# Kernel optimization log

Measured on AMD Instinct MI355X. Metric: run time of the kernel, lower is better.

The kernel has to match this reference:

```python
import jax, jax.numpy as jnp
import numpy as np

B, S, D, H = 2, 2048, 1024, 16
DK = D // H

def setup_inputs() -> dict:
    key = jax.random.key(0)
    ks = jax.random.split(key, 12)
    scale = 1.0 / np.sqrt(D)
    return {
        "q": jax.random.normal(ks[0], (B, S, D), jnp.float32),
        "k": jax.random.normal(ks[1], (B, S, D), jnp.float32),
        "v": jax.random.normal(ks[2], (B, S, D), jnp.float32),
        "mask": jax.random.randint(ks[3], (B, 1, S, S), 0, 2, jnp.int32),
        "w_q": jax.random.normal(ks[4], (D, D), jnp.float32) * scale,
        "b_q": jnp.zeros((D,), jnp.float32),
        "w_k": jax.random.normal(ks[5], (D, D), jnp.float32) * scale,
        "b_k": jnp.zeros((D,), jnp.float32),
        "w_v": jax.random.normal(ks[6], (D, D), jnp.float32) * scale,
        "b_v": jnp.zeros((D,), jnp.float32),
        "w_o": jax.random.normal(ks[7], (D, D), jnp.float32) * scale,
        "b_o": jnp.zeros((D,), jnp.float32),
    }

def reference(q, k, v, mask, w_q, b_q, w_k, b_k, w_v, b_v, w_o, b_o):
    # projections (nn.Linear: x @ W^T + b)
    Q = q @ w_q.T + b_q  # [B,S,D]
    K = k @ w_k.T + b_k
    V = v @ w_v.T + b_v
    # split heads -> [B,H,S,DK]
    Q = Q.reshape(B, S, H, DK).transpose(0, 2, 1, 3)
    K = K.reshape(B, S, H, DK).transpose(0, 2, 1, 3)
    V = V.reshape(B, S, H, DK).transpose(0, 2, 1, 3)
    scores = jnp.einsum("bhqd,bhkd->bhqk", Q, K) / jnp.sqrt(jnp.float32(DK))
    scores = jnp.where(mask == 0, jnp.float32(-1e9), scores)
    attn = jax.nn.softmax(scores, axis=-1)  # dropout p=0 -> identity
    x = jnp.einsum("bhqk,bhkd->bhqd", attn, V)
    x = x.transpose(0, 2, 1, 3).reshape(B, S, D)
    return x @ w_o.T + b_o
```

## Files before the change

### kernel.cpp

```cpp
#include <hip/hip_runtime.h>
#include <hip/hip_bf16.h>
#include <cstdint>
#include <cstddef>

typedef short bf16x8 __attribute__((ext_vector_type(8)));
typedef short bf16x4v __attribute__((ext_vector_type(4)));
typedef float f32x4 __attribute__((ext_vector_type(4)));
typedef __hip_bfloat16 bf16;

constexpr int Bb = 2, Ss = 2048, Dd = 1024, Hh = 16, DKk = 64;

__device__ __forceinline__ void async_lds16(void* lds, const void* g) {
  __builtin_amdgcn_global_load_lds(
      (const __attribute__((address_space(1))) void*)g,
      (__attribute__((address_space(3))) void*)lds, 16, 0, 0);
}

__device__ __forceinline__ float bf2f(bf16 x) { return __bfloat162float(x); }
__device__ __forceinline__ short f2bf(float x) {
  bf16 h = __float2bfloat16(x);
  return *(short*)&h;
}
__device__ __forceinline__ float bfs2f(short s) {
  return __uint_as_float(((uint32_t)(uint16_t)s) << 16);
}

struct CvtArgs {
  const float* src[12];
  short* dst[12];
  int n[12];
  int count;
};

__global__ __launch_bounds__(256)
void cvt_all(CvtArgs a)
{
  const int t = blockIdx.y;
  if (t >= a.count) return;
  const float* s = a.src[t];
  short* d = a.dst[t];
  const int n = a.n[t];
  const int stride = gridDim.x * blockDim.x * 4;
  for (int i = (blockIdx.x * blockDim.x + threadIdx.x) * 4; i < n; i += stride) {
    const float4 v = *(const float4*)(s + i);
    bf16x4v o;
    o[0] = f2bf(v.x); o[1] = f2bf(v.y); o[2] = f2bf(v.z); o[3] = f2bf(v.w);
    *(bf16x4v*)(d + i) = o;
  }
}

__global__ __launch_bounds__(256)
void pack_mask(const int* __restrict__ mask, uint32_t* __restrict__ bits)
{
  const int i = blockIdx.x * 256 + threadIdx.x;
  const unsigned long long bal = __ballot(mask[i] != 0);
  if ((threadIdx.x & 63) == 0)
    *(unsigned long long*)(bits + (i >> 5)) = bal;
}

__global__ __launch_bounds__(256, 2)
void gemm_bt(const bf16* __restrict__ A0, const bf16* __restrict__ A1, const bf16* __restrict__ A2,
             const bf16* __restrict__ W0, const bf16* __restrict__ W1, const bf16* __restrict__ W2,
             const bf16* __restrict__ b0, const bf16* __restrict__ b1, const bf16* __restrict__ b2,
             void* __restrict__ O0, void* __restrict__ O1, void* __restrict__ O2,
             float scale0, int wf32, int vtrans)
{
  extern __shared__ char smem[];
  const int mt  = blockIdx.x;
  const int by  = blockIdx.y;
  const int mat = by >> 3;
  const int nt  = by & 7;
  const bf16* A    = (mat == 0) ? A0 : (mat == 1) ? A1 : A2;
  const bf16* W    = (mat == 0) ? W0 : (mat == 1) ? W1 : W2;
  const bf16* bias = (mat == 0) ? b0 : (mat == 1) ? b1 : b2;
  void*       Out  = (mat == 0) ? O0 : (mat == 1) ? O1 : O2;
  const float scale = (mat == 0) ? scale0 : 1.0f;

  const int tid  = threadIdx.x;
  const int w    = tid >> 6;
  const int lane = tid & 63;
  const int quad = lane >> 4;
  const int l16  = lane & 15;
  const int wm   = (w & 1) * 64;
  const int wn   = (w >> 1) * 64;

  const int srow = lane >> 3;
  const int sseg = (lane & 7) ^ srow;

  const char* Abytes = (const char*)A;
  const char* Wbytes = (const char*)W;

  f32x4 acc[4][4];
#pragma unroll
  for (int i = 0; i < 4; ++i)
#pragma unroll
    for (int j = 0; j < 4; ++j) acc[i][j] = f32x4{0.f, 0.f, 0.f, 0.f};

  for (int kt = 0; kt < 16; ++kt) {
    __syncthreads();
#pragma unroll
    for (int c = 0; c < 4; ++c) {
      const int r0 = w * 32 + c * 8;
      async_lds16(smem + r0 * 128,
                  Abytes + (size_t)(mt * 128 + r0 + srow) * 2048 + kt * 128 + sseg * 16);
      async_lds16(smem + 16384 + r0 * 128,
                  Wbytes + (size_t)(nt * 128 + r0 + srow) * 2048 + kt * 128 + sseg * 16);
    }
    __syncthreads();
#pragma unroll
    for (int s = 0; s < 2; ++s) {
      bf16x8 af[4], bfg[4];
#pragma unroll
      for (int mb = 0; mb < 4; ++mb) {
        const int row = wm + mb * 16 + l16;
        af[mb] = *(const bf16x8*)(smem + row * 128 + (((4 * s + quad) ^ (row & 7)) * 16));
      }
#pragma unroll
      for (int nb = 0; nb < 4; ++nb) {
        const int row = wn + nb * 16 + l16;
        bfg[nb] = *(const bf16x8*)(smem + 16384 + row * 128 + (((4 * s + quad) ^ (row & 7)) * 16));
      }
#pragma unroll
      for (int mb = 0; mb < 4; ++mb)
#pragma unroll
        for (int nb = 0; nb < 4; ++nb)
          acc[mb][nb] = __builtin_amdgcn_mfma_f32_16x16x32_bf16(af[mb], bfg[nb], acc[mb][nb], 0, 0, 0);
    }
  }

  if (vtrans && mat == 2) {
    __syncthreads();
#pragma unroll
    for (int nb = 0; nb < 4; ++nb) {
      const int dk = wn + nb * 16 + l16;
      const float bv = bf2f(bias[nt * 128 + dk]);
#pragma unroll
      for (int mb = 0; mb < 4; ++mb) {
        const int s0 = wm + mb * 16 + quad * 4;
        bf16x4v pk;
#pragma unroll
        for (int r = 0; r < 4; ++r) pk[r] = f2bf(acc[mb][nb][r] + bv);
        *(bf16x4v*)(smem + dk * 256 + (((s0 >> 3) ^ (dk & 15)) * 16) + (s0 & 7) * 2) = pk;
      }
    }
    __syncthreads();
    const int bidx  = (mt * 128) >> 11;
    const int sbase = (mt * 128) & 2047;
#pragma unroll
    for (int i = 0; i < 8; ++i) {
      const int dk  = i * 16 + (tid >> 4);
      const int seg = tid & 15;
      bf16x8 vrow = *(const bf16x8*)(smem + dk * 256 + ((seg ^ (dk & 15)) * 16));
      *(bf16x8*)((bf16*)Out + (size_t)bidx * 2097152 + (size_t)(nt * 128 + dk) * 2048
                 + sbase + seg * 8) = vrow;
    }
  } else {
#pragma unroll
    for (int nb = 0; nb < 4; ++nb) {
      const int col = nt * 128 + wn + nb * 16 + l16;
      const float bv = bf2f(bias[col]);
#pragma unroll
      for (int mb = 0; mb < 4; ++mb) {
#pragma unroll
        for (int r = 0; r < 4; ++r) {
          const int row = mt * 128 + wm + mb * 16 + quad * 4 + r;
          const float val = (acc[mb][nb][r] + bv) * scale;
          const size_t idx = (size_t)row * 1024 + col;
          if (wf32) ((float*)Out)[idx] = val;
          else      ((bf16*)Out)[idx] = __float2bfloat16(val);
        }
      }
    }
  }
}

__global__ __launch_bounds__(256, 5)
void attn(const bf16* __restrict__ Qp, const bf16* __restrict__ Kp,
          const bf16* __restrict__ VpT, const uint32_t* __restrict__ mbits,
          bf16* __restrict__ Opart, float* __restrict__ Lpart)
{
  __shared__ char smem[32768];
  char* Pb = smem;
  char* Vt = smem + 16384;

  const int tile  = blockIdx.x;
  const int split = blockIdx.y;
  const int qt = tile & 31, h = (tile >> 5) & 15, b = tile >> 9;
  const int tid = threadIdx.x, w = tid >> 6, lane = tid & 63;
  const int quad = lane >> 4, l16 = lane & 15;
  const int qb = qt * 64;
  const size_t headoff = (size_t)b * (Ss * Dd) + h * DKk;
  const int qrow = qb + w * 16 + l16;

  bf16x8 qf[2];
#pragma unroll
  for (int s2 = 0; s2 < 2; ++s2)
    qf[s2] = *(const bf16x8*)(Qp + headoff + (size_t)qrow * Dd + s2 * 32 + quad * 8);

  f32x4 o[4];
  float Lacc = 0.f;
#pragma unroll
  for (int nbk = 0; nbk < 4; ++nbk) o[nbk] = f32x4{0.f, 0.f, 0.f, 0.f};

  const uint32_t* mrow = mbits + (size_t)(b * Ss + qrow) * 64;

  for (int kc = split * 8; kc < split * 8 + 8; ++kc) {
    const int kb = kc * 128;
    __syncthreads();
#pragma unroll
    for (int c = 0; c < 4; ++c) {
      {
        const int row = c * 32 + w * 8 + (lane >> 3);
        const int seg = (lane & 7) ^ (row & 7);
        async_lds16(Pb + c * 4096 + w * 1024,
                    Kp + headoff + (size_t)(kb + row) * Dd + seg * 8);
      }
      {
        const int row = c * 16 + w * 4 + (lane >> 4);
        const int seg = (lane & 15) ^ (row & 15);
        async_lds16(Vt + c * 4096 + w * 1024,
                    VpT + (size_t)b * 2097152 + (size_t)(h * 64 + row) * 2048 + kb + seg * 8);
      }
    }
    __syncthreads();

    f32x4 sc[8];
#pragma unroll
    for (int nb = 0; nb < 8; ++nb) sc[nb] = f32x4{0.f, 0.f, 0.f, 0.f};
#pragma unroll
    for (int s2 = 0; s2 < 2; ++s2)
#pragma unroll
      for (int nb = 0; nb < 8; ++nb) {
        const int row = nb * 16 + l16;
        bf16x8 kf = *(const bf16x8*)(Pb + row * 128 + (((s2 * 4 + quad) ^ (row & 7)) * 16));
        sc[nb] = __builtin_amdgcn_mfma_f32_16x16x32_bf16(kf, qf[s2], sc[nb], 0, 0, 0);
      }
    __syncthreads();

    const uint4 mwv = *(const uint4*)(mrow + kc * 4);
    const uint32_t mwa[4] = {mwv.x, mwv.y, mwv.z, mwv.w};
#pragma unroll
    for (int nb = 0; nb < 8; ++nb) {
      const uint32_t nib = (mwa[nb >> 1] >> ((nb & 1) * 16 + quad * 4)) & 0xFu;
      bf16x4v pk;
#pragma unroll
      for (int r = 0; r < 4; ++r) {
        const float p = (nib & (1u << r)) ? __expf(sc[nb][r]) : 0.0f;
        Lacc += p;
        pk[r] = f2bf(p);
      }
      *(bf16x4v*)(Pb + (size_t)(w * 16 + l16) * 256 +
                  (((2 * nb + (quad >> 1)) ^ l16) * 16) + (quad & 1) * 8) = pk;
    }
    asm volatile("s_waitcnt lgkmcnt(0)" ::: "memory");

#pragma unroll
    for (int kb4 = 0; kb4 < 2; ++kb4) {
      bf16x8 pf[2];
#pragma unroll
      for (int u = 0; u < 2; ++u)
        pf[u] = *(const bf16x8*)(Pb + (size_t)(w * 16 + l16) * 256 +
                                 (((kb4 * 8 + u * 4 + quad) ^ l16) * 16));
#pragma unroll
      for (int nbk = 0; nbk < 4; ++nbk) {
        const int row = nbk * 16 + l16;
#pragma unroll
        for (int u = 0; u < 2; ++u) {
          bf16x8 vf = *(const bf16x8*)(Vt + row * 256 +
                                       ((((kb4 * 2 + u) * 4 + quad) ^ (row & 15)) * 16));
          o[nbk] = __builtin_amdgcn_mfma_f32_16x16x32_bf16(pf[u], vf, o[nbk], 0, 0, 0);
        }
      }
    }
  }

  float Lq = Lacc;
  Lq += __shfl_xor(Lq, 16);
  Lq += __shfl_xor(Lq, 32);
  const size_t pbase = (size_t)(split * 1024 + tile) * 64;
#pragma unroll
  for (int r = 0; r < 4; ++r) {
    const int rr = w * 16 + quad * 4 + r;
#pragma unroll
    for (int nbk = 0; nbk < 4; ++nbk)
      Opart[(pbase + rr) * 64 + nbk * 16 + l16] = __float2bfloat16(o[nbk][r]);
  }
  if (quad == 0) Lpart[pbase + w * 16 + l16] = Lq;
}

__global__ __launch_bounds__(256)
void combine(const bf16* __restrict__ Opart, const float* __restrict__ Lpart,
             bf16* __restrict__ Xa)
{
  const int t = threadIdx.x;
  const int row = blockIdx.x * 32 + (t >> 3);
  const int dkc = (t & 7) * 8;
  const float L = Lpart[row] + Lpart[65536 + row];
  const float inv = 1.0f / L;
  const bf16x8 O0 = *(const bf16x8*)(Opart + (size_t)row * 64 + dkc);
  const bf16x8 O1 = *(const bf16x8*)(Opart + (size_t)(65536 + row) * 64 + dkc);
  bf16x8 res;
#pragma unroll
  for (int j = 0; j < 8; ++j)
    res[j] = f2bf((bfs2f(O0[j]) + bfs2f(O1[j])) * inv);
  const int tile = row >> 6, r64 = row & 63;
  const int b = tile >> 9, h = (tile >> 5) & 15, q = (tile & 31) * 64 + r64;
  *(bf16x8*)(Xa + (size_t)(b * 2048 + q) * 1024 + h * 64 + dkc) = res;
}

extern "C" void kernel_launch(void* const* d_in, const int* in_sizes, int n_in,
                              void* d_out, int out_size, void* d_ws, size_t ws_size,
                              hipStream_t stream)
{
  const float* q  = (const float*)d_in[0];
  const float* k  = (const float*)d_in[1];
  const float* v  = (const float*)d_in[2];
  const int*   mk = (const int*)d_in[3];
  const float* wq = (const float*)d_in[4];
  const float* bq = (const float*)d_in[5];
  const float* wk = (const float*)d_in[6];
  const float* bk = (const float*)d_in[7];
  const float* wv = (const float*)d_in[8];
  const float* bv = (const float*)d_in[9];
  const float* wo = (const float*)d_in[10];
  const float* bo = (const float*)d_in[11];
  float* out = (float*)d_out;

  char* ws = (char*)d_ws;
  bf16* qb_  = (bf16*)(ws + ((size_t)0  << 20));
  bf16* kb_  = (bf16*)(ws + ((size_t)8  << 20));
  bf16* vb_  = (bf16*)(ws + ((size_t)16 << 20));
  bf16* Qp   = (bf16*)(ws + ((size_t)24 << 20));
  bf16* Kp   = (bf16*)(ws + ((size_t)32 << 20));
  bf16* VpT  = (bf16*)(ws + ((size_t)40 << 20));
  bf16* wqb  = (bf16*)(ws + ((size_t)48 << 20));
  bf16* wkb  = (bf16*)(ws + ((size_t)50 << 20));
  bf16* wvb  = (bf16*)(ws + ((size_t)52 << 20));
  bf16* wob  = (bf16*)(ws + ((size_t)54 << 20));
  bf16* bqb  = (bf16*)(ws + ((size_t)56 << 20));
  bf16* bkb  = (bf16*)(ws + ((size_t)56 << 20) + 2048);
  bf16* bvb  = (bf16*)(ws + ((size_t)56 << 20) + 4096);
  bf16* bob  = (bf16*)(ws + ((size_t)56 << 20) + 6144);
  uint32_t* mbits = (uint32_t*)(ws + ((size_t)56 << 20) + 65536);
  bf16*  Opart = (bf16*)(ws + ((size_t)0 << 20));
  float* Lpart = (float*)(ws + ((size_t)16 << 20));
  bf16*  Xa    = (bf16*)(ws + ((size_t)17 << 20));

  const int NA = Bb * Ss * Dd;
  const int NW = Dd * Dd;

  CvtArgs ca;
  ca.src[0] = q;  ca.dst[0] = (short*)qb_; ca.n[0] = NA;
  ca.src[1] = k;  ca.dst[1] = (short*)kb_; ca.n[1] = NA;
  ca.src[2] = v;  ca.dst[2] = (short*)vb_; ca.n[2] = NA;
  ca.src[3] = wq; ca.dst[3] = (short*)wqb; ca.n[3] = NW;
  ca.src[4] = wk; ca.dst[4] = (short*)wkb; ca.n[4] = NW;
  ca.src[5] = wv; ca.dst[5] = (short*)wvb; ca.n[5] = NW;
  ca.src[6] = wo; ca.dst[6] = (short*)wob; ca.n[6] = NW;
  ca.src[7] = bq; ca.dst[7] = (short*)bqb; ca.n[7] = Dd;
  ca.src[8] = bk; ca.dst[8] = (short*)bkb; ca.n[8] = Dd;
  ca.src[9] = bv; ca.dst[9] = (short*)bvb; ca.n[9] = Dd;
  ca.src[10] = bo; ca.dst[10] = (short*)bob; ca.n[10] = Dd;
  ca.src[11] = bo; ca.dst[11] = (short*)bob; ca.n[11] = 0;
  ca.count = 11;

  dim3 blk(256);
  cvt_all<<<dim3(1024, 11), blk, 0, stream>>>(ca);
  pack_mask<<<dim3(Bb * Ss * Ss / 256), blk, 0, stream>>>(mk, mbits);

  gemm_bt<<<dim3(32, 24), blk, 32768, stream>>>(qb_, kb_, vb_, wqb, wkb, wvb,
                                                bqb, bkb, bvb,
                                                (void*)Qp, (void*)Kp, (void*)VpT,
                                                0.125f, 0, 1);
  attn<<<dim3(1024, 2), blk, 0, stream>>>(Qp, Kp, VpT, mbits, Opart, Lpart);
  combine<<<dim3(2048), blk, 0, stream>>>(Opart, Lpart, Xa);
  gemm_bt<<<dim3(32, 8), blk, 32768, stream>>>(Xa, Xa, Xa, wob, wob, wob,
                                               bob, bob, bob,
                                               (void*)out, (void*)out, (void*)out,
                                               1.0f, 1, 0);
}
```

Measured before the change: 296.7 us.

## Process 128 query rows per attention block with a three-way KV split

Each attention block now covers 128 query rows, with each wave handling two 16-row sets. Every K and V tile loaded into LDS therefore feeds twice as many MFMAs, and the key range is split three ways (6/5/5 chunks) instead of two. The combine kernel sums three partials, and the workspace is remapped to fit the larger partial buffers. The bf16 conversions now use a cheap add-and-shift rounding, and the gemm launch bounds allow three blocks per CU. The trade-off is more registers and more LDS per block (48KB), which lowers occupancy, plus a third partial to write and read.

```diff
diff --git a/kernel.cpp b/kernel.cpp
--- a/kernel.cpp
+++ b/kernel.cpp
@@ -20,6 +20,13 @@
 __device__ __forceinline__ short f2bf(float x) {
   bf16 h = __float2bfloat16(x);
   return *(short*)&h;
+}
+__device__ __forceinline__ short f2bf_fast(float x) {
+  return (short)((__float_as_uint(x) + 0x8000u) >> 16);
+}
+__device__ __forceinline__ uint32_t pack2bf(float a, float b) {
+  return ((__float_as_uint(a) + 0x8000u) >> 16) |
+         ((__float_as_uint(b) + 0x8000u) & 0xffff0000u);
 }
 __device__ __forceinline__ float bfs2f(short s) {
   return __uint_as_float(((uint32_t)(uint16_t)s) << 16);
@@ -58,7 +65,7 @@
     *(unsigned long long*)(bits + (i >> 5)) = bal;
 }
 
-__global__ __launch_bounds__(256, 2)
+__global__ __launch_bounds__(256, 3)
 void gemm_bt(const bf16* __restrict__ A0, const bf16* __restrict__ A1, const bf16* __restrict__ A2,
              const bf16* __restrict__ W0, const bf16* __restrict__ W1, const bf16* __restrict__ W2,
              const bf16* __restrict__ b0, const bf16* __restrict__ b1, const bf16* __restrict__ b2,
@@ -139,7 +146,7 @@
         const int s0 = wm + mb * 16 + quad * 4;
         bf16x4v pk;
 #pragma unroll
-        for (int r = 0; r < 4; ++r) pk[r] = f2bf(acc[mb][nb][r] + bv);
+        for (int r = 0; r < 4; ++r) pk[r] = f2bf_fast(acc[mb][nb][r] + bv);
         *(bf16x4v*)(smem + dk * 256 + (((s0 >> 3) ^ (dk & 15)) * 16) + (s0 & 7) * 2) = pk;
       }
     }
@@ -167,44 +174,57 @@
           const float val = (acc[mb][nb][r] + bv) * scale;
           const size_t idx = (size_t)row * 1024 + col;
           if (wf32) ((float*)Out)[idx] = val;
-          else      ((bf16*)Out)[idx] = __float2bfloat16(val);
+          else      ((bf16*)Out)[idx] = *(bf16*)&(short&)*(short[]){f2bf_fast(val)};
         }
       }
     }
   }
 }
 
-__global__ __launch_bounds__(256, 5)
+__global__ __launch_bounds__(256, 3)
 void attn(const bf16* __restrict__ Qp, const bf16* __restrict__ Kp,
           const bf16* __restrict__ VpT, const uint32_t* __restrict__ mbits,
           bf16* __restrict__ Opart, float* __restrict__ Lpart)
 {
-  __shared__ char smem[32768];
-  char* Pb = smem;
+  __shared__ char smem[49152];
+  char* Kb = smem;
   char* Vt = smem + 16384;
+  char* Ph = smem + 32768;
 
   const int tile  = blockIdx.x;
   const int split = blockIdx.y;
-  const int qt = tile & 31, h = (tile >> 5) & 15, b = tile >> 9;
+  const int qt = tile & 15, h = (tile >> 4) & 15, b = tile >> 8;
   const int tid = threadIdx.x, w = tid >> 6, lane = tid & 63;
   const int quad = lane >> 4, l16 = lane & 15;
-  const int qb = qt * 64;
+  const int qb = qt * 128;
   const size_t headoff = (size_t)b * (Ss * Dd) + h * DKk;
-  const int qrow = qb + w * 16 + l16;
-
-  bf16x8 qf[2];
-#pragma unroll
-  for (int s2 = 0; s2 < 2; ++s2)
-    qf[s2] = *(const bf16x8*)(Qp + headoff + (size_t)qrow * Dd + s2 * 32 + quad * 8);
-
-  f32x4 o[4];
-  float Lacc = 0.f;
-#pragma unroll
-  for (int nbk = 0; nbk < 4; ++nbk) o[nbk] = f32x4{0.f, 0.f, 0.f, 0.f};
-
-  const uint32_t* mrow = mbits + (size_t)(b * Ss + qrow) * 64;
-
-  for (int kc = split * 8; kc < split * 8 + 8; ++kc) {
+
+  const int kc0 = (split == 0) ? 0 : (split == 1) ? 6 : 11;
+  const int kc1 = (split == 0) ? 6 : (split == 1) ? 11 : 16;
+
+  bf16x8 qf[2][2];
+#pragma unroll
+  for (int set = 0; set < 2; ++set)
+#pragma unroll
+    for (int s2 = 0; s2 < 2; ++s2) {
+      const int row = qb + w * 32 + set * 16 + l16;
+      qf[set][s2] = *(const bf16x8*)(Qp + headoff + (size_t)row * Dd + s2 * 32 + quad * 8);
+    }
+
+  f32x4 o[2][4];
+  float Lacc[2] = {0.f, 0.f};
+#pragma unroll
+  for (int set = 0; set < 2; ++set)
+#pragma unroll
+    for (int nbk = 0; nbk < 4; ++nbk) o[set][nbk] = f32x4{0.f, 0.f, 0.f, 0.f};
+
+  const uint32_t* mrow0 = mbits + (size_t)(b * Ss + qb + w * 32 + l16) * 64;
+  const uint32_t* mrow1 = mrow0 + 16 * 64;
+
+  char* Preg = (w < 2) ? smem : Ph;
+  const int prowbase = (w & 1) * 32;
+
+  for (int kc = kc0; kc < kc1; ++kc) {
     const int kb = kc * 128;
     __syncthreads();
 #pragma unroll
@@ -212,7 +232,7 @@
       {
         const int row = c * 32 + w * 8 + (lane >> 3);
         const int seg = (lane & 7) ^ (row & 7);
-        async_lds16(Pb + c * 4096 + w * 1024,
+        async_lds16(Kb + c * 4096 + w * 1024,
                     Kp + headoff + (size_t)(kb + row) * Dd + seg * 8);
       }
       {
@@ -224,68 +244,81 @@
     }
     __syncthreads();
 
-    f32x4 sc[8];
-#pragma unroll
-    for (int nb = 0; nb < 8; ++nb) sc[nb] = f32x4{0.f, 0.f, 0.f, 0.f};
+    f32x4 sc[2][8];
+#pragma unroll
+    for (int set = 0; set < 2; ++set)
+#pragma unroll
+      for (int nb = 0; nb < 8; ++nb) sc[set][nb] = f32x4{0.f, 0.f, 0.f, 0.f};
 #pragma unroll
     for (int s2 = 0; s2 < 2; ++s2)
 #pragma unroll
       for (int nb = 0; nb < 8; ++nb) {
         const int row = nb * 16 + l16;
-        bf16x8 kf = *(const bf16x8*)(Pb + row * 128 + (((s2 * 4 + quad) ^ (row & 7)) * 16));
-        sc[nb] = __builtin_amdgcn_mfma_f32_16x16x32_bf16(kf, qf[s2], sc[nb], 0, 0, 0);
-      }
-    __syncthreads();
-
-    const uint4 mwv = *(const uint4*)(mrow + kc * 4);
-    const uint32_t mwa[4] = {mwv.x, mwv.y, mwv.z, mwv.w};
-#pragma unroll
-    for (int nb = 0; nb < 8; ++nb) {
-      const uint32_t nib = (mwa[nb >> 1] >> ((nb & 1) * 16 + quad * 4)) & 0xFu;
-      bf16x4v pk;
-#pragma unroll
-      for (int r = 0; r < 4; ++r) {
-        const float p = (nib & (1u << r)) ? __expf(sc[nb][r]) : 0.0f;
-        Lacc += p;
-        pk[r] = f2bf(p);
-      }
-      *(bf16x4v*)(Pb + (size_t)(w * 16 + l16) * 256 +
-                  (((2 * nb + (quad >> 1)) ^ l16) * 16) + (quad & 1) * 8) = pk;
+        bf16x8 kf = *(const bf16x8*)(Kb + row * 128 + (((s2 * 4 + quad) ^ (row & 7)) * 16));
+        sc[0][nb] = __builtin_amdgcn_mfma_f32_16x16x32_bf16(kf, qf[0][s2], sc[0][nb], 0, 0, 0);
+        sc[1][nb] = __builtin_amdgcn_mfma_f32_16x16x32_bf16(kf, qf[1][s2], sc[1][nb], 0, 0, 0);
+      }
+    __syncthreads();
+
+#pragma unroll
+    for (int set = 0; set < 2; ++set) {
+      const uint4 mwv = *(const uint4*)((set == 0 ? mrow0 : mrow1) + kc * 4);
+      const uint32_t mwa[4] = {mwv.x, mwv.y, mwv.z, mwv.w};
+      char* Prow = Preg + (size_t)(prowbase + set * 16 + l16) * 256;
+#pragma unroll
+      for (int nb = 0; nb < 8; ++nb) {
+        const uint32_t nib = (mwa[nb >> 1] >> ((nb & 1) * 16 + quad * 4)) & 0xFu;
+        const float p0 = (nib & 1u) ? __expf(sc[set][nb][0]) : 0.f;
+        const float p1 = (nib & 2u) ? __expf(sc[set][nb][1]) : 0.f;
+        const float p2 = (nib & 4u) ? __expf(sc[set][nb][2]) : 0.f;
+        const float p3 = (nib & 8u) ? __expf(sc[set][nb][3]) : 0.f;
+        Lacc[set] += (p0 + p1) + (p2 + p3);
+        uint2 pk;
+        pk.x = pack2bf(p0, p1);
+        pk.y = pack2bf(p2, p3);
+        *(uint2*)(Prow + (((2 * nb + (quad >> 1)) ^ l16) * 16) + (quad & 1) * 8) = pk;
+      }
     }
     asm volatile("s_waitcnt lgkmcnt(0)" ::: "memory");
 
 #pragma unroll
-    for (int kb4 = 0; kb4 < 2; ++kb4) {
-      bf16x8 pf[2];
-#pragma unroll
-      for (int u = 0; u < 2; ++u)
-        pf[u] = *(const bf16x8*)(Pb + (size_t)(w * 16 + l16) * 256 +
-                                 (((kb4 * 8 + u * 4 + quad) ^ l16) * 16));
+    for (int kb4 = 0; kb4 < 2; ++kb4)
+#pragma unroll
+      for (int u = 0; u < 2; ++u) {
+        bf16x8 pf[2];
+#pragma unroll
+        for (int set = 0; set < 2; ++set)
+          pf[set] = *(const bf16x8*)(Preg + (size_t)(prowbase + set * 16 + l16) * 256 +
+                                     (((kb4 * 8 + u * 4 + quad) ^ l16) * 16));
+#pragma unroll
+        for (int nbk = 0; nbk < 4; ++nbk) {
+          const int row = nbk * 16 + l16;
+          bf16x8 vf = *(const bf16x8*)(Vt + row * 256 +
+                                       (((kb4 * 8 + u * 4 + quad) ^ (row & 15)) * 16));
+          o[0][nbk] = __builtin_amdgcn_mfma_f32_16x16x32_bf16(pf[0], vf, o[0][nbk], 0, 0, 0);
+          o[1][nbk] = __builtin_amdgcn_mfma_f32_16x16x32_bf16(pf[1], vf, o[1][nbk], 0, 0, 0);
+        }
+      }
+  }
+
+#pragma unroll
+  for (int set = 0; set < 2; ++set) {
+    float Lq = Lacc[set];
+    Lq += __shfl_xor(Lq, 16);
+    Lq += __shfl_xor(Lq, 32);
+    const int rbase = tile * 128 + w * 32 + set * 16;
+#pragma unroll
+    for (int r = 0; r < 4; ++r) {
+      const int rglob = rbase + quad * 4 + r;
 #pragma unroll
       for (int nbk = 0; nbk < 4; ++nbk) {
-        const int row = nbk * 16 + l16;
-#pragma unroll
-        for (int u = 0; u < 2; ++u) {
-          bf16x8 vf = *(const bf16x8*)(Vt + row * 256 +
-                                       ((((kb4 * 2 + u) * 4 + quad) ^ (row & 15)) * 16));
-          o[nbk] = __builtin_amdgcn_mfma_f32_16x16x32_bf16(pf[u], vf, o[nbk], 0, 0, 0);
-        }
-      }
-    }
+        short s = f2bf_fast(o[set][nbk][r]);
+        ((short*)Opart)[((size_t)split * 65536 + rglob) * 64 + nbk * 16 + l16] = s;
+      }
+    }
+    if (quad == 0)
+      Lpart[(size_t)split * 65536 + rbase + l16] = Lq;
   }
-
-  float Lq = Lacc;
-  Lq += __shfl_xor(Lq, 16);
-  Lq += __shfl_xor(Lq, 32);
-  const size_t pbase = (size_t)(split * 1024 + tile) * 64;
-#pragma unroll
-  for (int r = 0; r < 4; ++r) {
-    const int rr = w * 16 + quad * 4 + r;
-#pragma unroll
-    for (int nbk = 0; nbk < 4; ++nbk)
-      Opart[(pbase + rr) * 64 + nbk * 16 + l16] = __float2bfloat16(o[nbk][r]);
-  }
-  if (quad == 0) Lpart[pbase + w * 16 + l16] = Lq;
 }
 
 __global__ __launch_bounds__(256)
@@ -295,16 +328,17 @@
   const int t = threadIdx.x;
   const int row = blockIdx.x * 32 + (t >> 3);
   const int dkc = (t & 7) * 8;
-  const float L = Lpart[row] + Lpart[65536 + row];
+  const float L = Lpart[row] + Lpart[65536 + row] + Lpart[131072 + row];
   const float inv = 1.0f / L;
   const bf16x8 O0 = *(const bf16x8*)(Opart + (size_t)row * 64 + dkc);
-  const bf16x8 O1 = *(const bf16x8*)(Opart + (size_t)(65536 + row) * 64 + dkc);
+  const bf16x8 O1 = *(const bf16x8*)(Opart + ((size_t)65536 + row) * 64 + dkc);
+  const bf16x8 O2 = *(const bf16x8*)(Opart + ((size_t)131072 + row) * 64 + dkc);
   bf16x8 res;
 #pragma unroll
   for (int j = 0; j < 8; ++j)
-    res[j] = f2bf((bfs2f(O0[j]) + bfs2f(O1[j])) * inv);
-  const int tile = row >> 6, r64 = row & 63;
-  const int b = tile >> 9, h = (tile >> 5) & 15, q = (tile & 31) * 64 + r64;
+    res[j] = f2bf_fast((bfs2f(O0[j]) + bfs2f(O1[j]) + bfs2f(O2[j])) * inv);
+  const int tile = row >> 7, qlocal = row & 127;
+  const int b = tile >> 8, h = (tile >> 4) & 15, q = (tile & 15) * 128 + qlocal;
   *(bf16x8*)(Xa + (size_t)(b * 2048 + q) * 1024 + h * 64 + dkc) = res;
 }
 
@@ -343,8 +377,8 @@
   bf16* bob  = (bf16*)(ws + ((size_t)56 << 20) + 6144);
   uint32_t* mbits = (uint32_t*)(ws + ((size_t)56 << 20) + 65536);
   bf16*  Opart = (bf16*)(ws + ((size_t)0 << 20));
-  float* Lpart = (float*)(ws + ((size_t)16 << 20));
-  bf16*  Xa    = (bf16*)(ws + ((size_t)17 << 20));
+  float* Lpart = (float*)(ws + ((size_t)48 << 20));
+  bf16*  Xa    = (bf16*)(ws + ((size_t)24 << 20));
 
   const int NA = Bb * Ss * Dd;
   const int NW = Dd * Dd;
@@ -372,7 +406,7 @@
                                                 bqb, bkb, bvb,
                                                 (void*)Qp, (void*)Kp, (void*)VpT,
                                                 0.125f, 0, 1);
-  attn<<<dim3(1024, 2), blk, 0, stream>>>(Qp, Kp, VpT, mbits, Opart, Lpart);
+  attn<<<dim3(512, 3), blk, 0, stream>>>(Qp, Kp, VpT, mbits, Opart, Lpart);
   combine<<<dim3(2048), blk, 0, stream>>>(Opart, Lpart, Xa);
   gemm_bt<<<dim3(32, 8), blk, 32768, stream>>>(Xa, Xa, Xa, wob, wob, wob,
                                                bob, bob, bob,
```

New measurement: 281.5 us. -5.1%, faster.
